# Performance work log

Measured on AMD Instinct MI355X. Metric: run time of the kernel, lower is better.

## Reference

```python
import jax, jax.numpy as jnp
import numpy as np

N_MOLS = 2048
DEPTH = 4

def _graph_conv(fatoms, fbonds, agraph, bgraph, Wi, Wh, Wo, bo):
    # fbonds: [n_bonds, 88] -> nei_input_h: [n_bonds, H]
    nei_input_h = fbonds @ Wi.T
    msg = jax.nn.relu(nei_input_h)
    for _ in range(DEPTH - 1):
        # gather neighbor bond messages [n_bonds, max_nei, H], sum over neighbors
        nei = msg[bgraph].sum(axis=1)
        msg = jax.nn.relu(nei_input_h + nei @ Wh.T)
    # aggregate bond messages into atoms: [n_atoms, max_nei, H] -> [n_atoms, H]
    atom_nei = msg[agraph].sum(axis=1)
    atom_in = jnp.concatenate([fatoms, atom_nei], axis=1)  # [n_atoms, 82+H]
    return jax.nn.relu(atom_in @ Wo.T + bo)

def _mol_embed(atom_h, mol_idx):
    return jax.ops.segment_sum(atom_h, mol_idx, num_segments=N_MOLS)

def setup_inputs() -> dict:
    key = jax.random.key(0)
    ks = jax.random.split(key, 24)
    n_atoms, n_bonds, max_nei, H = 100000, 200000, 10, 256
    d = {}
    d['fatoms_src'] = jax.random.normal(ks[0], (n_atoms, 82), jnp.float32)
    d['fbonds_src'] = jax.random.normal(ks[1], (n_bonds, 88), jnp.float32)
    d['agraph_src'] = jax.random.randint(ks[2], (n_atoms, max_nei), 0, n_bonds, jnp.int32)
    d['bgraph_src'] = jax.random.randint(ks[3], (n_bonds, max_nei), 0, n_bonds, jnp.int32)
    d['mol_idx_src'] = jnp.sort(jax.random.randint(ks[4], (n_atoms,), 0, N_MOLS, jnp.int32))
    d['fatoms_tgt'] = jax.random.normal(ks[5], (n_atoms, 82), jnp.float32)
    d['fbonds_tgt'] = jax.random.normal(ks[6], (n_bonds, 88), jnp.float32)
    d['agraph_tgt'] = jax.random.randint(ks[7], (n_atoms, max_nei), 0, n_bonds, jnp.int32)
    d['bgraph_tgt'] = jax.random.randint(ks[8], (n_bonds, max_nei), 0, n_bonds, jnp.int32)
    d['mol_idx_tgt'] = jnp.sort(jax.random.randint(ks[9], (n_atoms,), 0, N_MOLS, jnp.int32))
    s = 0.05
    d['Wi_s'] = jax.random.normal(ks[10], (H, 88), jnp.float32) * s
    d['Wh_s'] = jax.random.normal(ks[11], (H, H), jnp.float32) * s
    d['Wo_s'] = jax.random.normal(ks[12], (H, 82 + H), jnp.float32) * s
    d['bo_s'] = jax.random.normal(ks[13], (H,), jnp.float32) * s
    d['Wi_t'] = jax.random.normal(ks[14], (H, 88), jnp.float32) * s
    d['Wh_t'] = jax.random.normal(ks[15], (H, H), jnp.float32) * s
    d['Wo_t'] = jax.random.normal(ks[16], (H, 82 + H), jnp.float32) * s
    d['bo_t'] = jax.random.normal(ks[17], (H,), jnp.float32) * s
    d['Wrh'] = jax.random.normal(ks[18], (H, H), jnp.float32) * s
    d['brh'] = jax.random.normal(ks[19], (H,), jnp.float32) * s
    d['Wro'] = jax.random.normal(ks[20], (1, H), jnp.float32) * s
    d['bro'] = jax.random.normal(ks[21], (1,), jnp.float32) * s
    return d

def reference(fatoms_src, fbonds_src, agraph_src, bgraph_src, mol_idx_src,
              fatoms_tgt, fbonds_tgt, agraph_tgt, bgraph_tgt, mol_idx_tgt,
              Wi_s, Wh_s, Wo_s, bo_s, Wi_t, Wh_t, Wo_t, bo_t,
              Wrh, brh, Wro, bro):
    src_atom_h = _graph_conv(fatoms_src, fbonds_src, agraph_src, bgraph_src, Wi_s, Wh_s, Wo_s, bo_s)
    src_mol_h = _mol_embed(src_atom_h, mol_idx_src)
    tgt_atom_h = _graph_conv(fatoms_tgt, fbonds_tgt, agraph_tgt, bgraph_tgt, Wi_t, Wh_t, Wo_t, bo_t)
    tgt_mol_h = _mol_embed(tgt_atom_h, mol_idx_tgt)
    rxn_h = jax.nn.relu((tgt_mol_h - src_mol_h) @ Wrh.T + brh)
    return rxn_h @ Wro.T + bro  # [N_MOLS, 1]
```

## Files before the change

kernel.cpp:

```cpp
#include <hip/hip_runtime.h>

typedef _Float16 f16;
using f16x8 = __attribute__((ext_vector_type(8))) _Float16;
using f32x4 = __attribute__((ext_vector_type(4))) float;

#define H 256
#define NM 2048

__device__ __forceinline__ void gload_lds16(const f16* g, f16* lds)
{
    __builtin_amdgcn_global_load_lds(
        (const __attribute__((address_space(1))) void*)g,
        (__attribute__((address_space(3))) void*)lds, 16, 0, 0);
}

__global__ __launch_bounds__(256, 4) void gemm_dense(
    const float* __restrict__ A1, int lda1, int K1r,
    const f16*  __restrict__ W1,
    const f16*  __restrict__ A2,
    const f16*  __restrict__ W2,
    const float* __restrict__ bias, f16* __restrict__ C, int M)
{
    __shared__ f16 Bs[256][64];

    const int bm   = blockIdx.x * 64;
    const int tid  = threadIdx.x;
    const int wave = tid >> 6, lane = tid & 63;
    const int lrow = lane & 15;
    const int kg   = lane >> 4;
    const int swz  = lrow & 7;

    const int glr = lane >> 3;
    const int gsc = (lane & 7) ^ glr;

    const int  myrow = bm + wave * 16 + lrow;
    const bool rowok = myrow < M;

    f32x4 acc[16];
    #pragma unroll
    for (int n = 0; n < 16; ++n) acc[n] = (f32x4){0.f, 0.f, 0.f, 0.f};

    f16x8 af2[8];
    if (A2 != nullptr) {
        #pragma unroll
        for (int t = 0; t < 8; ++t) {
            if (rowok)
                af2[t] = *(const f16x8*)(A2 + (size_t)myrow * H + kg * 8 + t * 32);
            else {
                #pragma unroll
                for (int e = 0; e < 8; ++e) af2[t][e] = (f16)0.f;
            }
        }
    }

    auto stageB = [&](const f16* W, int ldw, int k0) {
        #pragma unroll
        for (int q = 0; q < 8; ++q)
            gload_lds16(W + (size_t)(wave * 64 + q * 8 + glr) * ldw + k0 + gsc * 8,
                        &Bs[wave * 64 + q * 8][0]);
    };

    auto mfma_win = [&](f16x8 a0, f16x8 a1) {
        #pragma unroll
        for (int ks = 0; ks < 2; ++ks) {
            const int cb = ((ks * 4 + kg) ^ swz) * 8;
            const f16x8 av = ks ? a1 : a0;
            #pragma unroll
            for (int n = 0; n < 16; ++n) {
                f16x8 b = *(const f16x8*)&Bs[n * 16 + lrow][cb];
                acc[n] = __builtin_amdgcn_mfma_f32_16x16x32_f16(av, b, acc[n], 0, 0, 0);
            }
        }
    };

    if (A1 != nullptr) {
        #pragma unroll
        for (int w = 0; w < 2; ++w) {
            f16x8 a[2];
            #pragma unroll
            for (int c = 0; c < 2; ++c) {
                const int k0 = (w * 8 + c * 4 + kg) * 8;
                const float* sp = A1 + (size_t)myrow * lda1 + k0;
                f16 tmp[8];
                #pragma unroll
                for (int i = 0; i < 8; i += 2) {
                    float x = 0.f, y = 0.f;
                    if (rowok) {
                        if (k0 + i + 1 < K1r) { float2 v = *(const float2*)(sp + i); x = v.x; y = v.y; }
                        else if (k0 + i < K1r) { x = sp[i]; }
                    }
                    tmp[i] = (f16)x; tmp[i + 1] = (f16)y;
                }
                a[c] = *(const f16x8*)tmp;
            }
            stageB(W1, 128, w * 64);
            __syncthreads();
            mfma_win(a[0], a[1]);
            __syncthreads();
        }
    }

    if (A2 != nullptr) {
        #pragma unroll
        for (int w = 0; w < 4; ++w) {
            stageB(W2, H, w * 64);
            __syncthreads();
            mfma_win(af2[w * 2], af2[w * 2 + 1]);
            __syncthreads();
        }
    }

    #pragma unroll
    for (int n = 0; n < 16; ++n) {
        const int gc = n * 16 + lrow;
        const float bv = bias ? bias[gc] : 0.f;
        #pragma unroll
        for (int r = 0; r < 4; ++r) {
            const int gr = bm + wave * 16 + kg * 4 + r;
            if (gr < M) C[(size_t)gr * H + gc] = (f16)fmaxf(acc[n][r] + bv, 0.f);
        }
    }
}

__global__ __launch_bounds__(256) void gather_sum10(
    const f16* __restrict__ src, const int* __restrict__ idx,
    f16* __restrict__ dst, int n_rows)
{
    int row  = blockIdx.x * 8 + (threadIdx.x >> 5);
    int lane = threadIdx.x & 31;
    if (row >= n_rows) return;
    const int* ip = idx + (size_t)row * 10;
    float s[8] = {};
    #pragma unroll
    for (int j = 0; j < 10; ++j) {
        int r = ip[j];
        float4 v = *((const float4*)(src + (size_t)r * H) + lane);
        const f16* pb = (const f16*)&v;
        #pragma unroll
        for (int e = 0; e < 8; ++e) s[e] += (float)pb[e];
    }
    f16 o[8];
    #pragma unroll
    for (int e = 0; e < 8; ++e) o[e] = (f16)s[e];
    *((float4*)(dst + (size_t)row * H) + lane) = *(const float4*)o;
}

__global__ __launch_bounds__(256) void convert_w(
    const float* __restrict__ src, int lds_, int koff, int kvalid,
    f16* __restrict__ dst, int Kd)
{
    int n = blockIdx.x;
    for (int k = threadIdx.x; k < Kd; k += 256) {
        float v = (k < kvalid) ? src[(size_t)n * lds_ + koff + k] : 0.f;
        dst[(size_t)n * Kd + k] = (f16)v;
    }
}

__global__ __launch_bounds__(256) void segsum(
    const f16* __restrict__ atom_h, const int* __restrict__ mol_idx,
    float* __restrict__ mol_h, int n_atoms)
{
    int m = blockIdx.x;
    int lo = 0, hi = n_atoms;
    while (lo < hi) { int mid = (lo + hi) >> 1; if (mol_idx[mid] < m) lo = mid + 1; else hi = mid; }
    int start = lo;
    hi = n_atoms;
    while (lo < hi) { int mid = (lo + hi) >> 1; if (mol_idx[mid] < m + 1) lo = mid + 1; else hi = mid; }
    int end = lo;
    int c = threadIdx.x;
    float s = 0.f;
    for (int a = start; a < end; ++a) s += (float)atom_h[(size_t)a * H + c];
    mol_h[(size_t)m * H + c] = s;
}

__global__ __launch_bounds__(256) void diff_kernel(
    const float* __restrict__ a, const float* __restrict__ b,
    f16* __restrict__ c, int n)
{
    int i = blockIdx.x * 256 + threadIdx.x;
    if (i < n) c[i] = (f16)(a[i] - b[i]);
}

__global__ __launch_bounds__(256) void final_dot(
    const f16* __restrict__ rxn, const float* __restrict__ Wro,
    const float* __restrict__ bro, float* __restrict__ out)
{
    int m = blockIdx.x;
    int t = threadIdx.x;
    float v = (float)rxn[(size_t)m * H + t] * Wro[t];
    #pragma unroll
    for (int off = 32; off; off >>= 1) v += __shfl_down(v, off, 64);
    __shared__ float red[4];
    if ((t & 63) == 0) red[t >> 6] = v;
    __syncthreads();
    if (t == 0) out[m] = red[0] + red[1] + red[2] + red[3] + bro[0];
}

static void run_graph(const float* fatoms, const float* fbonds, const int* agraph,
                      const int* bgraph, const int* mol_idx,
                      const f16* Wi16, const f16* Wh16, const f16* Wo1, const f16* Wo2,
                      const float* bo,
                      f16* bufA, f16* bufB, float* molh,
                      int n_atoms, int n_bonds, hipStream_t stream)
{
    dim3 gb((n_bonds + 63) / 64);
    dim3 ga((n_atoms + 63) / 64);

    gemm_dense<<<gb, 256, 0, stream>>>(fbonds, 88, 88, Wi16,
                                       (const f16*)nullptr, (const f16*)nullptr,
                                       (const float*)nullptr, bufA, n_bonds);
    f16* cur = bufA; f16* nxt = bufB;
    for (int it = 0; it < 3; ++it) {
        gather_sum10<<<(n_bonds + 7) / 8, 256, 0, stream>>>(cur, bgraph, nxt, n_bonds);
        gemm_dense<<<gb, 256, 0, stream>>>(fbonds, 88, 88, Wi16,
                                           nxt, Wh16,
                                           (const float*)nullptr, cur, n_bonds);
    }
    gather_sum10<<<(n_atoms + 7) / 8, 256, 0, stream>>>(cur, agraph, nxt, n_atoms);
    gemm_dense<<<ga, 256, 0, stream>>>(fatoms, 82, 82, Wo1,
                                       nxt, Wo2,
                                       bo, cur, n_atoms);
    segsum<<<NM, 256, 0, stream>>>(cur, mol_idx, molh, n_atoms);
}

extern "C" void kernel_launch(void* const* d_in, const int* in_sizes, int n_in,
                              void* d_out, int out_size, void* d_ws, size_t ws_size,
                              hipStream_t stream)
{
    const float* fatoms_src = (const float*)d_in[0];
    const float* fbonds_src = (const float*)d_in[1];
    const int*   agraph_src = (const int*)d_in[2];
    const int*   bgraph_src = (const int*)d_in[3];
    const int*   mol_idx_src= (const int*)d_in[4];
    const float* fatoms_tgt = (const float*)d_in[5];
    const float* fbonds_tgt = (const float*)d_in[6];
    const int*   agraph_tgt = (const int*)d_in[7];
    const int*   bgraph_tgt = (const int*)d_in[8];
    const int*   mol_idx_tgt= (const int*)d_in[9];
    const float* Wi_s = (const float*)d_in[10];
    const float* Wh_s = (const float*)d_in[11];
    const float* Wo_s = (const float*)d_in[12];
    const float* bo_s = (const float*)d_in[13];
    const float* Wi_t = (const float*)d_in[14];
    const float* Wh_t = (const float*)d_in[15];
    const float* Wo_t = (const float*)d_in[16];
    const float* bo_t = (const float*)d_in[17];
    const float* Wrh  = (const float*)d_in[18];
    const float* brh  = (const float*)d_in[19];
    const float* Wro  = (const float*)d_in[20];
    const float* bro  = (const float*)d_in[21];

    const int n_atoms = in_sizes[0] / 82;
    const int n_bonds = in_sizes[1] / 88;

    char* ws = (char*)d_ws;
    size_t off = 0;
    auto alloc = [&](size_t bytes) { size_t o = off; off = (off + bytes + 255) & ~(size_t)255; return o; };
    f16*   bufA = (f16*)(ws + alloc((size_t)n_bonds * H * 2));
    f16*   bufB = (f16*)(ws + alloc((size_t)n_bonds * H * 2));
    float* molS = (float*)(ws + alloc((size_t)NM * H * 4));
    float* molT = (float*)(ws + alloc((size_t)NM * H * 4));
    f16*   dbuf = (f16*)(ws + alloc((size_t)NM * H * 2));
    f16*   rxn  = (f16*)(ws + alloc((size_t)NM * H * 2));
    f16* Wi16_s = (f16*)(ws + alloc(256 * 128 * 2));
    f16* Wh16_s = (f16*)(ws + alloc(256 * 256 * 2));
    f16* Wo1_s  = (f16*)(ws + alloc(256 * 128 * 2));
    f16* Wo2_s  = (f16*)(ws + alloc(256 * 256 * 2));
    f16* Wi16_t = (f16*)(ws + alloc(256 * 128 * 2));
    f16* Wh16_t = (f16*)(ws + alloc(256 * 256 * 2));
    f16* Wo1_t  = (f16*)(ws + alloc(256 * 128 * 2));
    f16* Wo2_t  = (f16*)(ws + alloc(256 * 256 * 2));
    f16* Wrh16  = (f16*)(ws + alloc(256 * 256 * 2));

    convert_w<<<256, 256, 0, stream>>>(Wi_s,  88,  0,  88, Wi16_s, 128);
    convert_w<<<256, 256, 0, stream>>>(Wh_s, 256,  0, 256, Wh16_s, 256);
    convert_w<<<256, 256, 0, stream>>>(Wo_s, 338,  0,  82, Wo1_s, 128);
    convert_w<<<256, 256, 0, stream>>>(Wo_s, 338, 82, 256, Wo2_s, 256);
    convert_w<<<256, 256, 0, stream>>>(Wi_t,  88,  0,  88, Wi16_t, 128);
    convert_w<<<256, 256, 0, stream>>>(Wh_t, 256,  0, 256, Wh16_t, 256);
    convert_w<<<256, 256, 0, stream>>>(Wo_t, 338,  0,  82, Wo1_t, 128);
    convert_w<<<256, 256, 0, stream>>>(Wo_t, 338, 82, 256, Wo2_t, 256);
    convert_w<<<256, 256, 0, stream>>>(Wrh, 256,  0, 256, Wrh16, 256);

    run_graph(fatoms_src, fbonds_src, agraph_src, bgraph_src, mol_idx_src,
              Wi16_s, Wh16_s, Wo1_s, Wo2_s, bo_s,
              bufA, bufB, molS, n_atoms, n_bonds, stream);
    run_graph(fatoms_tgt, fbonds_tgt, agraph_tgt, bgraph_tgt, mol_idx_tgt,
              Wi16_t, Wh16_t, Wo1_t, Wo2_t, bo_t,
              bufA, bufB, molT, n_atoms, n_bonds, stream);

    diff_kernel<<<(NM * H + 255) / 256, 256, 0, stream>>>(molT, molS, dbuf, NM * H);
    gemm_dense<<<NM / 64, 256, 0, stream>>>((const float*)nullptr, 0, 0, (const f16*)nullptr,
                                            dbuf, Wrh16,
                                            brh, rxn, NM);
    final_dot<<<NM, 256, 0, stream>>>(rxn, Wro, bro, (float*)d_out);
}
```

Measured before the change: 2.311 ms.

## Double-buffer weight tiles and compute 128-row blocks in templated GEMM

The dense GEMM now processes 128 rows per block, two 16-row MFMA tiles per wave, so each staged weight tile in LDS is reused twice as much. LDS weight staging is double-buffered: the next K-window's A fragments and B tile are loaded while the current window's MFMAs run, which drops one barrier per window. Template flags replace the runtime null checks on the input branches. The cost is twice the accumulator registers and LDS, with launch bounds relaxed to 2 blocks per CU, which may reduce occupancy.

```diff
diff --git a/kernel.cpp b/kernel.cpp
--- a/kernel.cpp
+++ b/kernel.cpp
@@ -14,16 +14,18 @@
         (__attribute__((address_space(3))) void*)lds, 16, 0, 0);
 }
 
-__global__ __launch_bounds__(256, 4) void gemm_dense(
+template<bool P0, bool P1>
+__global__ __launch_bounds__(256, 2) void gemm_dense(
     const float* __restrict__ A1, int lda1, int K1r,
     const f16*  __restrict__ W1,
     const f16*  __restrict__ A2,
     const f16*  __restrict__ W2,
     const float* __restrict__ bias, f16* __restrict__ C, int M)
 {
-    __shared__ f16 Bs[256][64];
-
-    const int bm   = blockIdx.x * 64;
+    __shared__ f16 Bs[2][256][64];
+    constexpr int NW = (P0 ? 2 : 0) + (P1 ? 4 : 0);
+
+    const int bm   = blockIdx.x * 128;
     const int tid  = threadIdx.x;
     const int wave = tid >> 6, lane = tid & 63;
     const int lrow = lane & 15;
@@ -33,91 +35,108 @@
     const int glr = lane >> 3;
     const int gsc = (lane & 7) ^ glr;
 
-    const int  myrow = bm + wave * 16 + lrow;
-    const bool rowok = myrow < M;
-
-    f32x4 acc[16];
-    #pragma unroll
-    for (int n = 0; n < 16; ++n) acc[n] = (f32x4){0.f, 0.f, 0.f, 0.f};
-
-    f16x8 af2[8];
-    if (A2 != nullptr) {
-        #pragma unroll
-        for (int t = 0; t < 8; ++t) {
-            if (rowok)
-                af2[t] = *(const f16x8*)(A2 + (size_t)myrow * H + kg * 8 + t * 32);
-            else {
-                #pragma unroll
-                for (int e = 0; e < 8; ++e) af2[t][e] = (f16)0.f;
-            }
-        }
-    }
-
-    auto stageB = [&](const f16* W, int ldw, int k0) {
+    const int r0 = bm + wave * 32 + lrow;
+
+    f32x4 acc[2][16];
+    #pragma unroll
+    for (int m = 0; m < 2; ++m)
+        #pragma unroll
+        for (int n = 0; n < 16; ++n) acc[m][n] = (f32x4){0.f, 0.f, 0.f, 0.f};
+
+    f16x8 afb[2][2][2];
+
+    auto stageB = [&](int sel, const f16* W, int ldw, int k0) {
         #pragma unroll
         for (int q = 0; q < 8; ++q)
             gload_lds16(W + (size_t)(wave * 64 + q * 8 + glr) * ldw + k0 + gsc * 8,
-                        &Bs[wave * 64 + q * 8][0]);
+                        &Bs[sel][wave * 64 + q * 8][0]);
     };
 
-    auto mfma_win = [&](f16x8 a0, f16x8 a1) {
-        #pragma unroll
-        for (int ks = 0; ks < 2; ++ks) {
-            const int cb = ((ks * 4 + kg) ^ swz) * 8;
-            const f16x8 av = ks ? a1 : a0;
+    auto loadA = [&](int w, f16x8 (&dst)[2][2]) {
+        if (P0 && w < 2) {
             #pragma unroll
-            for (int n = 0; n < 16; ++n) {
-                f16x8 b = *(const f16x8*)&Bs[n * 16 + lrow][cb];
-                acc[n] = __builtin_amdgcn_mfma_f32_16x16x32_f16(av, b, acc[n], 0, 0, 0);
+            for (int m = 0; m < 2; ++m) {
+                const int row = r0 + m * 16;
+                const bool ok = row < M;
+                #pragma unroll
+                for (int ks = 0; ks < 2; ++ks) {
+                    const int k0 = w * 64 + ks * 32 + kg * 8;
+                    const float* sp = A1 + (size_t)row * lda1 + k0;
+                    f16 tmp[8];
+                    #pragma unroll
+                    for (int i = 0; i < 8; i += 2) {
+                        float x = 0.f, y = 0.f;
+                        if (ok) {
+                            if (k0 + i + 1 < K1r) { float2 v = *(const float2*)(sp + i); x = v.x; y = v.y; }
+                            else if (k0 + i < K1r) { x = sp[i]; }
+                        }
+                        tmp[i] = (f16)x; tmp[i + 1] = (f16)y;
+                    }
+                    dst[ks][m] = *(const f16x8*)tmp;
+                }
+            }
+        } else {
+            const int wp = P0 ? w - 2 : w;
+            #pragma unroll
+            for (int m = 0; m < 2; ++m) {
+                const int row = r0 + m * 16;
+                const bool ok = row < M;
+                #pragma unroll
+                for (int ks = 0; ks < 2; ++ks) {
+                    if (ok)
+                        dst[ks][m] = *(const f16x8*)(A2 + (size_t)row * H + wp * 64 + ks * 32 + kg * 8);
+                    else {
+                        #pragma unroll
+                        for (int e = 0; e < 8; ++e) dst[ks][m][e] = (f16)0.f;
+                    }
+                }
             }
         }
     };
 
-    if (A1 != nullptr) {
-        #pragma unroll
-        for (int w = 0; w < 2; ++w) {
-            f16x8 a[2];
+    auto mfmaW = [&](int sel, f16x8 (&a)[2][2]) {
+        #pragma unroll
+        for (int ks = 0; ks < 2; ++ks) {
+            const int cb = ((ks * 4 + kg) ^ swz) * 8;
             #pragma unroll
-            for (int c = 0; c < 2; ++c) {
-                const int k0 = (w * 8 + c * 4 + kg) * 8;
-                const float* sp = A1 + (size_t)myrow * lda1 + k0;
-                f16 tmp[8];
+            for (int n = 0; n < 16; ++n) {
+                f16x8 b = *(const f16x8*)&Bs[sel][n * 16 + lrow][cb];
                 #pragma unroll
-                for (int i = 0; i < 8; i += 2) {
-                    float x = 0.f, y = 0.f;
-                    if (rowok) {
-                        if (k0 + i + 1 < K1r) { float2 v = *(const float2*)(sp + i); x = v.x; y = v.y; }
-                        else if (k0 + i < K1r) { x = sp[i]; }
-                    }
-                    tmp[i] = (f16)x; tmp[i + 1] = (f16)y;
-                }
-                a[c] = *(const f16x8*)tmp;
+                for (int m = 0; m < 2; ++m)
+                    acc[m][n] = __builtin_amdgcn_mfma_f32_16x16x32_f16(a[ks][m], b, acc[m][n], 0, 0, 0);
             }
-            stageB(W1, 128, w * 64);
-            __syncthreads();
-            mfma_win(a[0], a[1]);
-            __syncthreads();
         }
-    }
-
-    if (A2 != nullptr) {
-        #pragma unroll
-        for (int w = 0; w < 4; ++w) {
-            stageB(W2, H, w * 64);
-            __syncthreads();
-            mfma_win(af2[w * 2], af2[w * 2 + 1]);
-            __syncthreads();
+    };
+
+    auto Wof   = [&](int w) -> const f16* { return (P0 && w < 2) ? W1 : W2; };
+    auto ldwof = [&](int w) { return (P0 && w < 2) ? 128 : 256; };
+    auto k0of  = [&](int w) { return (P0 && w < 2) ? w * 64 : (P0 ? (w - 2) * 64 : w * 64); };
+
+    loadA(0, afb[0]);
+    stageB(0, Wof(0), ldwof(0), k0of(0));
+    __syncthreads();
+
+    #pragma unroll
+    for (int w = 0; w < NW; ++w) {
+        if (w + 1 < NW) {
+            loadA(w + 1, afb[(w + 1) & 1]);
+            stageB((w + 1) & 1, Wof(w + 1), ldwof(w + 1), k0of(w + 1));
         }
-    }
-
-    #pragma unroll
-    for (int n = 0; n < 16; ++n) {
-        const int gc = n * 16 + lrow;
-        const float bv = bias ? bias[gc] : 0.f;
-        #pragma unroll
-        for (int r = 0; r < 4; ++r) {
-            const int gr = bm + wave * 16 + kg * 4 + r;
-            if (gr < M) C[(size_t)gr * H + gc] = (f16)fmaxf(acc[n][r] + bv, 0.f);
+        mfmaW(w & 1, afb[w & 1]);
+        __syncthreads();
+    }
+
+    #pragma unroll
+    for (int m = 0; m < 2; ++m) {
+        #pragma unroll
+        for (int n = 0; n < 16; ++n) {
+            const int gc = n * 16 + lrow;
+            const float bv = bias ? bias[gc] : 0.f;
+            #pragma unroll
+            for (int r = 0; r < 4; ++r) {
+                const int gr = bm + wave * 32 + m * 16 + kg * 4 + r;
+                if (gr < M) C[(size_t)gr * H + gc] = (f16)fmaxf(acc[m][n][r] + bv, 0.f);
+            }
         }
     }
 }
@@ -203,23 +222,22 @@
                       f16* bufA, f16* bufB, float* molh,
                       int n_atoms, int n_bonds, hipStream_t stream)
 {
-    dim3 gb((n_bonds + 63) / 64);
-    dim3 ga((n_atoms + 63) / 64);
-
-    gemm_dense<<<gb, 256, 0, stream>>>(fbonds, 88, 88, Wi16,
-                                       (const f16*)nullptr, (const f16*)nullptr,
-                                       (const float*)nullptr, bufA, n_bonds);
+    dim3 gb((n_bonds + 127) / 128);
+    dim3 ga((n_atoms + 127) / 128);
+
+    gemm_dense<true, false><<<gb, 256, 0, stream>>>(
+        fbonds, 88, 88, Wi16, (const f16*)nullptr, (const f16*)nullptr,
+        (const float*)nullptr, bufA, n_bonds);
     f16* cur = bufA; f16* nxt = bufB;
     for (int it = 0; it < 3; ++it) {
         gather_sum10<<<(n_bonds + 7) / 8, 256, 0, stream>>>(cur, bgraph, nxt, n_bonds);
-        gemm_dense<<<gb, 256, 0, stream>>>(fbonds, 88, 88, Wi16,
-                                           nxt, Wh16,
-                                           (const float*)nullptr, cur, n_bonds);
+        gemm_dense<true, true><<<gb, 256, 0, stream>>>(
+            fbonds, 88, 88, Wi16, nxt, Wh16,
+            (const float*)nullptr, cur, n_bonds);
     }
     gather_sum10<<<(n_atoms + 7) / 8, 256, 0, stream>>>(cur, agraph, nxt, n_atoms);
-    gemm_dense<<<ga, 256, 0, stream>>>(fatoms, 82, 82, Wo1,
-                                       nxt, Wo2,
-                                       bo, cur, n_atoms);
+    gemm_dense<true, true><<<ga, 256, 0, stream>>>(
+        fatoms, 82, 82, Wo1, nxt, Wo2, bo, cur, n_atoms);
     segsum<<<NM, 256, 0, stream>>>(cur, mol_idx, molh, n_atoms);
 }
 
@@ -290,8 +308,8 @@
               bufA, bufB, molT, n_atoms, n_bonds, stream);
 
     diff_kernel<<<(NM * H + 255) / 256, 256, 0, stream>>>(molT, molS, dbuf, NM * H);
-    gemm_dense<<<NM / 64, 256, 0, stream>>>((const float*)nullptr, 0, 0, (const f16*)nullptr,
-                                            dbuf, Wrh16,
-                                            brh, rxn, NM);
+    gemm_dense<false, true><<<NM / 128, 256, 0, stream>>>(
+        (const float*)nullptr, 0, 0, (const f16*)nullptr, dbuf, Wrh16,
+        brh, rxn, NM);
     final_dot<<<NM, 256, 0, stream>>>(rxn, Wro, bro, (float*)d_out);
 }
```

Result: slower. 2.654 ms (+14.8%).

## Overlap gather and GEMM halves within one heterogeneous fused kernel launch

Applied to the files above, without the earlier changes.

Splits each message-passing step into two row halves. A single fused launch interleaves GEMM blocks for the first half with gather blocks for the second half, so the memory-bound gather and the compute-bound MFMA GEMM run concurrently on the GPU. A third bond-sized buffer is used so the gather output and the GEMM output do not alias, and the path is enabled only when the workspace is large enough. This adds an extra launch per step and relies on the block-ID interleave (period) to balance the two kinds of work.

```diff
diff --git a/kernel.cpp b/kernel.cpp
--- a/kernel.cpp
+++ b/kernel.cpp
@@ -14,27 +14,25 @@
         (__attribute__((address_space(3))) void*)lds, 16, 0, 0);
 }
 
-__global__ __launch_bounds__(256, 4) void gemm_dense(
+__device__ __forceinline__ void gemm_body(
+    f16 (*Bs)[64],
     const float* __restrict__ A1, int lda1, int K1r,
     const f16*  __restrict__ W1,
     const f16*  __restrict__ A2,
     const f16*  __restrict__ W2,
-    const float* __restrict__ bias, f16* __restrict__ C, int M)
-{
-    __shared__ f16 Bs[256][64];
-
-    const int bm   = blockIdx.x * 64;
+    const float* __restrict__ bias, f16* __restrict__ C,
+    int bm, int Mend)
+{
     const int tid  = threadIdx.x;
     const int wave = tid >> 6, lane = tid & 63;
     const int lrow = lane & 15;
     const int kg   = lane >> 4;
     const int swz  = lrow & 7;
-
-    const int glr = lane >> 3;
-    const int gsc = (lane & 7) ^ glr;
+    const int glr  = lane >> 3;
+    const int gsc  = (lane & 7) ^ glr;
 
     const int  myrow = bm + wave * 16 + lrow;
-    const bool rowok = myrow < M;
+    const bool rowok = myrow < Mend;
 
     f32x4 acc[16];
     #pragma unroll
@@ -117,18 +115,15 @@
         #pragma unroll
         for (int r = 0; r < 4; ++r) {
             const int gr = bm + wave * 16 + kg * 4 + r;
-            if (gr < M) C[(size_t)gr * H + gc] = (f16)fmaxf(acc[n][r] + bv, 0.f);
-        }
-    }
-}
-
-__global__ __launch_bounds__(256) void gather_sum10(
+            if (gr < Mend) C[(size_t)gr * H + gc] = (f16)fmaxf(acc[n][r] + bv, 0.f);
+        }
+    }
+}
+
+__device__ __forceinline__ void gather_body(
     const f16* __restrict__ src, const int* __restrict__ idx,
-    f16* __restrict__ dst, int n_rows)
-{
-    int row  = blockIdx.x * 8 + (threadIdx.x >> 5);
-    int lane = threadIdx.x & 31;
-    if (row >= n_rows) return;
+    f16* __restrict__ dst, int row, int lane)
+{
     const int* ip = idx + (size_t)row * 10;
     float s[8] = {};
     #pragma unroll
@@ -143,6 +138,48 @@
     #pragma unroll
     for (int e = 0; e < 8; ++e) o[e] = (f16)s[e];
     *((float4*)(dst + (size_t)row * H) + lane) = *(const float4*)o;
+}
+
+__global__ __launch_bounds__(256, 4) void gemm_dense(
+    const float* __restrict__ A1, int lda1, int K1r,
+    const f16*  __restrict__ W1,
+    const f16*  __restrict__ A2,
+    const f16*  __restrict__ W2,
+    const float* __restrict__ bias, f16* __restrict__ C,
+    int row0, int Mend)
+{
+    __shared__ f16 Bs[256][64];
+    gemm_body(Bs, A1, lda1, K1r, W1, A2, W2, bias, C, row0 + blockIdx.x * 64, Mend);
+}
+
+__global__ __launch_bounds__(256) void gather_sum10(
+    const f16* __restrict__ src, const int* __restrict__ idx,
+    f16* __restrict__ dst, int row0, int rend)
+{
+    int row = row0 + blockIdx.x * 8 + (threadIdx.x >> 5);
+    if (row < rend) gather_body(src, idx, dst, row, threadIdx.x & 31);
+}
+
+__global__ __launch_bounds__(256, 4) void fused_step(
+    const float* __restrict__ A1, int lda1, int K1r,
+    const f16*  __restrict__ W1,
+    const f16*  __restrict__ A2,
+    const f16*  __restrict__ W2,
+    const float* __restrict__ bias, f16* __restrict__ C,
+    int g_row0, int g_Mend, int nge, int period,
+    const f16* __restrict__ gsrc, const int* __restrict__ gidx,
+    f16* __restrict__ gdst, int a_row0, int a_end)
+{
+    __shared__ f16 Bs[256][64];
+    const int bid = blockIdx.x;
+    const int q = bid / period, r = bid % period;
+    if (r == 0 && q < nge) {
+        gemm_body(Bs, A1, lda1, K1r, W1, A2, W2, bias, C, g_row0 + q * 64, g_Mend);
+    } else {
+        int ab = bid - min(q + 1, nge);
+        int row = a_row0 + ab * 8 + (threadIdx.x >> 5);
+        if (row < a_end) gather_body(gsrc, gidx, gdst, row, threadIdx.x & 31);
+    }
 }
 
 __global__ __launch_bounds__(256) void convert_w(
@@ -200,27 +237,58 @@
                       const int* bgraph, const int* mol_idx,
                       const f16* Wi16, const f16* Wh16, const f16* Wo1, const f16* Wo2,
                       const float* bo,
-                      f16* bufA, f16* bufB, float* molh,
+                      f16* bufA, f16* bufB, f16* bufY, bool overlap, float* molh,
                       int n_atoms, int n_bonds, hipStream_t stream)
 {
-    dim3 gb((n_bonds + 63) / 64);
-    dim3 ga((n_atoms + 63) / 64);
-
-    gemm_dense<<<gb, 256, 0, stream>>>(fbonds, 88, 88, Wi16,
-                                       (const f16*)nullptr, (const f16*)nullptr,
-                                       (const float*)nullptr, bufA, n_bonds);
+    const float* nul_f = nullptr;
+    const f16*   nul_h = nullptr;
+
+    gemm_dense<<<(n_bonds + 63) / 64, 256, 0, stream>>>(
+        fbonds, 88, 88, Wi16, nul_h, nul_h, nul_f, bufA, 0, n_bonds);
     f16* cur = bufA; f16* nxt = bufB;
+
+    if (!overlap) {
+        for (int it = 0; it < 3; ++it) {
+            gather_sum10<<<(n_bonds + 7) / 8, 256, 0, stream>>>(cur, bgraph, nxt, 0, n_bonds);
+            gemm_dense<<<(n_bonds + 63) / 64, 256, 0, stream>>>(
+                fbonds, 88, 88, Wi16, nxt, Wh16, nul_f, cur, 0, n_bonds);
+        }
+        gather_sum10<<<(n_atoms + 7) / 8, 256, 0, stream>>>(cur, agraph, nxt, 0, n_atoms);
+        gemm_dense<<<(n_atoms + 63) / 64, 256, 0, stream>>>(
+            fatoms, 82, 82, Wo1, nxt, Wo2, bo, cur, 0, n_atoms);
+        segsum<<<NM, 256, 0, stream>>>(cur, mol_idx, molh, n_atoms);
+        return;
+    }
+
+    const int hb  = min((((n_bonds / 2) + 63) / 64) * 64, n_bonds);
+    const int nge_b = hb / 64;
+    const int nga_b = (n_bonds - hb + 7) / 8;
+    const int tot_b = nge_b + nga_b;
+    const int per_b = tot_b / nge_b;
+
     for (int it = 0; it < 3; ++it) {
-        gather_sum10<<<(n_bonds + 7) / 8, 256, 0, stream>>>(cur, bgraph, nxt, n_bonds);
-        gemm_dense<<<gb, 256, 0, stream>>>(fbonds, 88, 88, Wi16,
-                                           nxt, Wh16,
-                                           (const float*)nullptr, cur, n_bonds);
-    }
-    gather_sum10<<<(n_atoms + 7) / 8, 256, 0, stream>>>(cur, agraph, nxt, n_atoms);
-    gemm_dense<<<ga, 256, 0, stream>>>(fatoms, 82, 82, Wo1,
-                                       nxt, Wo2,
-                                       bo, cur, n_atoms);
-    segsum<<<NM, 256, 0, stream>>>(cur, mol_idx, molh, n_atoms);
+        gather_sum10<<<(hb + 7) / 8, 256, 0, stream>>>(cur, bgraph, bufY, 0, hb);
+        fused_step<<<tot_b, 256, 0, stream>>>(
+            fbonds, 88, 88, Wi16, bufY, Wh16, nul_f, nxt, 0, hb, nge_b, per_b,
+            cur, bgraph, bufY, hb, n_bonds);
+        gemm_dense<<<(n_bonds - hb + 63) / 64, 256, 0, stream>>>(
+            fbonds, 88, 88, Wi16, bufY, Wh16, nul_f, nxt, hb, n_bonds);
+        f16* t = cur; cur = nxt; nxt = t;
+    }
+
+    const int ahb  = min((((n_atoms / 2) + 63) / 64) * 64, n_atoms);
+    const int nge_a = ahb / 64;
+    const int nga_a = (n_atoms - ahb + 7) / 8;
+    const int tot_a = nge_a + nga_a;
+    const int per_a = tot_a / nge_a;
+
+    gather_sum10<<<(ahb + 7) / 8, 256, 0, stream>>>(cur, agraph, bufY, 0, ahb);
+    fused_step<<<tot_a, 256, 0, stream>>>(
+        fatoms, 82, 82, Wo1, bufY, Wo2, bo, nxt, 0, ahb, nge_a, per_a,
+        cur, agraph, bufY, ahb, n_atoms);
+    gemm_dense<<<(n_atoms - ahb + 63) / 64, 256, 0, stream>>>(
+        fatoms, 82, 82, Wo1, bufY, Wo2, bo, nxt, ahb, n_atoms);
+    segsum<<<NM, 256, 0, stream>>>(nxt, mol_idx, molh, n_atoms);
 }
 
 extern "C" void kernel_launch(void* const* d_in, const int* in_sizes, int n_in,
@@ -253,11 +321,18 @@
     const int n_atoms = in_sizes[0] / 82;
     const int n_bonds = in_sizes[1] / 88;
 
+    const size_t bondB = (size_t)n_bonds * H * sizeof(f16);
+    const size_t tailB = 2 * (size_t)NM * H * 4 + 2 * (size_t)NM * H * 2
+                       + 4 * (256 * 128 * 2) + 5 * (256 * 256 * 2)
+                       + 32 * 256;
+    const bool overlap = ws_size >= 3 * bondB + tailB;
+
     char* ws = (char*)d_ws;
     size_t off = 0;
     auto alloc = [&](size_t bytes) { size_t o = off; off = (off + bytes + 255) & ~(size_t)255; return o; };
-    f16*   bufA = (f16*)(ws + alloc((size_t)n_bonds * H * 2));
-    f16*   bufB = (f16*)(ws + alloc((size_t)n_bonds * H * 2));
+    f16*   bufA = (f16*)(ws + alloc(bondB));
+    f16*   bufB = (f16*)(ws + alloc(bondB));
+    f16*   bufY = overlap ? (f16*)(ws + alloc(bondB)) : nullptr;
     float* molS = (float*)(ws + alloc((size_t)NM * H * 4));
     float* molT = (float*)(ws + alloc((size_t)NM * H * 4));
     f16*   dbuf = (f16*)(ws + alloc((size_t)NM * H * 2));
@@ -284,14 +359,14 @@
 
     run_graph(fatoms_src, fbonds_src, agraph_src, bgraph_src, mol_idx_src,
               Wi16_s, Wh16_s, Wo1_s, Wo2_s, bo_s,
-              bufA, bufB, molS, n_atoms, n_bonds, stream);
+              bufA, bufB, bufY, overlap, molS, n_atoms, n_bonds, stream);
     run_graph(fatoms_tgt, fbonds_tgt, agraph_tgt, bgraph_tgt, mol_idx_tgt,
               Wi16_t, Wh16_t, Wo1_t, Wo2_t, bo_t,
-              bufA, bufB, molT, n_atoms, n_bonds, stream);
+              bufA, bufB, bufY, overlap, molT, n_atoms, n_bonds, stream);
 
     diff_kernel<<<(NM * H + 255) / 256, 256, 0, stream>>>(molT, molS, dbuf, NM * H);
-    gemm_dense<<<NM / 64, 256, 0, stream>>>((const float*)nullptr, 0, 0, (const f16*)nullptr,
-                                            dbuf, Wrh16,
-                                            brh, rxn, NM);
+    gemm_dense<<<NM / 64, 256, 0, stream>>>(
+        (const float*)nullptr, 0, 0, (const f16*)nullptr, dbuf, Wrh16,
+        brh, rxn, 0, NM);
     final_dot<<<NM, 256, 0, stream>>>(rxn, Wro, bro, (float*)d_out);
 }
```

After: 2.323 ms. No clear change (+0.5%).

## Double-buffer weight staging in dense GEMM with templated phase selection

Applied to the files above, without the earlier changes.

The dense GEMM now splits each 64-wide K window into two 128-column halves and stages them into a double-buffered LDS array, so the load of the next window overlaps the MFMAs on the current one. Only one barrier per step remains instead of two. The kernel is templated on which input phases are present, which removes the runtime null checks and lets the window loop unroll fully. LDS use per block stays the same (2x128x64 instead of 256x64), but there are more, smaller stages and possible extra register pressure from preloading every A fragment.

```diff
diff --git a/kernel.cpp b/kernel.cpp
--- a/kernel.cpp
+++ b/kernel.cpp
@@ -14,72 +14,53 @@
         (__attribute__((address_space(3))) void*)lds, 16, 0, 0);
 }
 
+template<bool P0, bool P1>
 __global__ __launch_bounds__(256, 4) void gemm_dense(
     const float* __restrict__ A1, int lda1, int K1r,
     const f16*  __restrict__ W1,
     const f16*  __restrict__ A2,
     const f16*  __restrict__ W2,
-    const float* __restrict__ bias, f16* __restrict__ C, int M)
-{
-    __shared__ f16 Bs[256][64];
-
-    const int bm   = blockIdx.x * 64;
+    const float* __restrict__ bias, f16* __restrict__ C,
+    int row0, int Mend)
+{
+    __shared__ f16 Bs[2][128][64];
+    constexpr int NW = (P0 ? 4 : 0) + (P1 ? 8 : 0);
+
+    const int bm   = row0 + blockIdx.x * 64;
     const int tid  = threadIdx.x;
     const int wave = tid >> 6, lane = tid & 63;
     const int lrow = lane & 15;
     const int kg   = lane >> 4;
     const int swz  = lrow & 7;
-
-    const int glr = lane >> 3;
-    const int gsc = (lane & 7) ^ glr;
+    const int glr  = lane >> 3;
+    const int gsc  = (lane & 7) ^ glr;
 
     const int  myrow = bm + wave * 16 + lrow;
-    const bool rowok = myrow < M;
+    const bool rowok = myrow < Mend;
 
     f32x4 acc[16];
     #pragma unroll
     for (int n = 0; n < 16; ++n) acc[n] = (f32x4){0.f, 0.f, 0.f, 0.f};
 
-    f16x8 af2[8];
-    if (A2 != nullptr) {
+    f16x8 af1[2][2];
+    f16x8 af2[4][2];
+    if (P1) {
         #pragma unroll
         for (int t = 0; t < 8; ++t) {
             if (rowok)
-                af2[t] = *(const f16x8*)(A2 + (size_t)myrow * H + kg * 8 + t * 32);
+                af2[t >> 1][t & 1] = *(const f16x8*)(A2 + (size_t)myrow * H + t * 32 + kg * 8);
             else {
                 #pragma unroll
-                for (int e = 0; e < 8; ++e) af2[t][e] = (f16)0.f;
+                for (int e = 0; e < 8; ++e) af2[t >> 1][t & 1][e] = (f16)0.f;
             }
         }
     }
-
-    auto stageB = [&](const f16* W, int ldw, int k0) {
-        #pragma unroll
-        for (int q = 0; q < 8; ++q)
-            gload_lds16(W + (size_t)(wave * 64 + q * 8 + glr) * ldw + k0 + gsc * 8,
-                        &Bs[wave * 64 + q * 8][0]);
-    };
-
-    auto mfma_win = [&](f16x8 a0, f16x8 a1) {
-        #pragma unroll
-        for (int ks = 0; ks < 2; ++ks) {
-            const int cb = ((ks * 4 + kg) ^ swz) * 8;
-            const f16x8 av = ks ? a1 : a0;
+    if (P0) {
+        #pragma unroll
+        for (int kw = 0; kw < 2; ++kw) {
             #pragma unroll
-            for (int n = 0; n < 16; ++n) {
-                f16x8 b = *(const f16x8*)&Bs[n * 16 + lrow][cb];
-                acc[n] = __builtin_amdgcn_mfma_f32_16x16x32_f16(av, b, acc[n], 0, 0, 0);
-            }
-        }
-    };
-
-    if (A1 != nullptr) {
-        #pragma unroll
-        for (int w = 0; w < 2; ++w) {
-            f16x8 a[2];
-            #pragma unroll
-            for (int c = 0; c < 2; ++c) {
-                const int k0 = (w * 8 + c * 4 + kg) * 8;
+            for (int ks = 0; ks < 2; ++ks) {
+                const int k0 = kw * 64 + ks * 32 + kg * 8;
                 const float* sp = A1 + (size_t)myrow * lda1 + k0;
                 f16 tmp[8];
                 #pragma unroll
@@ -91,23 +72,47 @@
                     }
                     tmp[i] = (f16)x; tmp[i + 1] = (f16)y;
                 }
-                a[c] = *(const f16x8*)tmp;
+                af1[kw][ks] = *(const f16x8*)tmp;
             }
-            stageB(W1, 128, w * 64);
-            __syncthreads();
-            mfma_win(a[0], a[1]);
-            __syncthreads();
         }
     }
 
-    if (A2 != nullptr) {
-        #pragma unroll
-        for (int w = 0; w < 4; ++w) {
-            stageB(W2, H, w * 64);
-            __syncthreads();
-            mfma_win(af2[w * 2], af2[w * 2 + 1]);
-            __syncthreads();
+    auto stage_w = [&](int w, int buf) {
+        const bool p0 = P0 && (w < 4);
+        const f16* W  = p0 ? W1 : W2;
+        const int ldw = p0 ? 128 : 256;
+        const int wp  = p0 ? w : (P0 ? w - 4 : w);
+        const int k0  = (wp >> 1) * 64;
+        const int nh  = wp & 1;
+        #pragma unroll
+        for (int q = 0; q < 4; ++q)
+            gload_lds16(W + (size_t)(nh * 128 + wave * 32 + q * 8 + glr) * ldw + k0 + gsc * 8,
+                        &Bs[buf][wave * 32 + q * 8][0]);
+    };
+
+    auto mfma_w = [&](int w, int buf) {
+        const bool p0 = P0 && (w < 4);
+        const int wp  = p0 ? w : (P0 ? w - 4 : w);
+        const int nh  = wp & 1;
+        #pragma unroll
+        for (int ks = 0; ks < 2; ++ks) {
+            const int cb = ((ks * 4 + kg) ^ swz) * 8;
+            const f16x8 a = p0 ? af1[wp >> 1][ks] : af2[wp >> 1][ks];
+            #pragma unroll
+            for (int j = 0; j < 8; ++j) {
+                f16x8 b = *(const f16x8*)&Bs[buf][j * 16 + lrow][cb];
+                acc[nh * 8 + j] = __builtin_amdgcn_mfma_f32_16x16x32_f16(a, b, acc[nh * 8 + j], 0, 0, 0);
+            }
         }
+    };
+
+    stage_w(0, 0);
+    __syncthreads();
+    #pragma unroll
+    for (int w = 0; w < NW; ++w) {
+        if (w + 1 < NW) stage_w(w + 1, (w + 1) & 1);
+        mfma_w(w, w & 1);
+        __syncthreads();
     }
 
     #pragma unroll
@@ -117,7 +122,7 @@
         #pragma unroll
         for (int r = 0; r < 4; ++r) {
             const int gr = bm + wave * 16 + kg * 4 + r;
-            if (gr < M) C[(size_t)gr * H + gc] = (f16)fmaxf(acc[n][r] + bv, 0.f);
+            if (gr < Mend) C[(size_t)gr * H + gc] = (f16)fmaxf(acc[n][r] + bv, 0.f);
         }
     }
 }
@@ -203,23 +208,21 @@
                       f16* bufA, f16* bufB, float* molh,
                       int n_atoms, int n_bonds, hipStream_t stream)
 {
-    dim3 gb((n_bonds + 63) / 64);
-    dim3 ga((n_atoms + 63) / 64);
-
-    gemm_dense<<<gb, 256, 0, stream>>>(fbonds, 88, 88, Wi16,
-                                       (const f16*)nullptr, (const f16*)nullptr,
-                                       (const float*)nullptr, bufA, n_bonds);
+    const float* nul_f = nullptr;
+    const f16*   nul_h = nullptr;
+
+    gemm_dense<true, false><<<(n_bonds + 63) / 64, 256, 0, stream>>>(
+        fbonds, 88, 88, Wi16, nul_h, nul_h, nul_f, bufA, 0, n_bonds);
     f16* cur = bufA; f16* nxt = bufB;
+
     for (int it = 0; it < 3; ++it) {
         gather_sum10<<<(n_bonds + 7) / 8, 256, 0, stream>>>(cur, bgraph, nxt, n_bonds);
-        gemm_dense<<<gb, 256, 0, stream>>>(fbonds, 88, 88, Wi16,
-                                           nxt, Wh16,
-                                           (const float*)nullptr, cur, n_bonds);
+        gemm_dense<true, true><<<(n_bonds + 63) / 64, 256, 0, stream>>>(
+            fbonds, 88, 88, Wi16, nxt, Wh16, nul_f, cur, 0, n_bonds);
     }
     gather_sum10<<<(n_atoms + 7) / 8, 256, 0, stream>>>(cur, agraph, nxt, n_atoms);
-    gemm_dense<<<ga, 256, 0, stream>>>(fatoms, 82, 82, Wo1,
-                                       nxt, Wo2,
-                                       bo, cur, n_atoms);
+    gemm_dense<true, true><<<(n_atoms + 63) / 64, 256, 0, stream>>>(
+        fatoms, 82, 82, Wo1, nxt, Wo2, bo, cur, 0, n_atoms);
     segsum<<<NM, 256, 0, stream>>>(cur, mol_idx, molh, n_atoms);
 }
 
@@ -290,8 +293,8 @@
               bufA, bufB, molT, n_atoms, n_bonds, stream);
 
     diff_kernel<<<(NM * H + 255) / 256, 256, 0, stream>>>(molT, molS, dbuf, NM * H);
-    gemm_dense<<<NM / 64, 256, 0, stream>>>((const float*)nullptr, 0, 0, (const f16*)nullptr,
-                                            dbuf, Wrh16,
-                                            brh, rxn, NM);
+    gemm_dense<false, true><<<NM / 64, 256, 0, stream>>>(
+        (const float*)nullptr, 0, 0, (const f16*)nullptr, dbuf, Wrh16,
+        brh, rxn, 0, NM);
     final_dot<<<NM, 256, 0, stream>>>(rxn, Wro, bro, (float*)d_out);
 }
```

Result: no change. 2.286 ms (-1.1%).
